# Kernel optimization log

Measured on AMD Instinct MI355X. Metric: run time of the kernel, lower is better.

## Reference

```python
import jax, jax.numpy as jnp
import numpy as np

B, H, S, D = 2, 12, 2048, 64


def setup_inputs() -> dict:
    key = jax.random.key(0)
    kq, kk, kv = jax.random.split(key, 3)
    q = jax.random.normal(kq, (B, H, S, D), dtype=jnp.float32)
    k = jax.random.normal(kk, (B, H, S, D), dtype=jnp.float32)
    v = jax.random.normal(kv, (B, H, S, D), dtype=jnp.float32)
    # causal mask: True = attend (keep), lower triangle
    mask = jnp.tril(jnp.ones((S, S), dtype=bool))
    return {"q": q, "k": k, "v": v, "mask": mask}


def reference(q, k, v, mask):
    dim = q.shape[-1]
    # [B,H,S,S] scores
    scores = jnp.einsum("bhqd,bhkd->bhqk", q, k) / jnp.sqrt(jnp.asarray(dim, q.dtype))
    # dynamic mask-direction logic from the original module:
    # if the mask is denser in the strict upper triangle, True means "mask out";
    # otherwise True means "keep".
    sq = mask.shape[-1]
    sample = mask.reshape(-1, sq, sq)[0]
    upper = jnp.triu(jnp.ones_like(sample, dtype=bool), k=1)
    flip = jnp.sum(sample & upper) > jnp.sum(sample & ~upper)
    keep = jnp.where(flip, ~mask, mask)  # True = keep
    neg_inf = jnp.asarray(-jnp.inf, scores.dtype)
    scores = jnp.where(keep, scores, neg_inf)
    weights = jax.nn.softmax(scores, axis=-1)
    # dropout with p_drop=0.0 is the identity
    return jnp.einsum("bhqk,bhkd->bhqd", weights, v)
```

## Files before the change

kernel.cpp:

```cpp
#include <hip/hip_runtime.h>
#include <hip/hip_bf16.h>


#define SEQ 2048
#define DH 64
#define NHEADS 24
#define BN 64
#define LDK 72
#define NSLOT (NHEADS * 16 * 4)
#define WS_FA14  ((size_t)NSLOT * 8192 * 2 + (size_t)NSLOT * 128 * 4)

typedef float f32x4 __attribute__((ext_vector_type(4)));
typedef __bf16 bf16x8 __attribute__((ext_vector_type(8)));
typedef __bf16 bf16x4 __attribute__((ext_vector_type(4)));

#if __has_builtin(__builtin_amdgcn_exp2f)
#define EXP2F(x) __builtin_amdgcn_exp2f(x)
#else
#define EXP2F(x) exp2f(x)
#endif

#define QSCALE 0.1803368801111204f

__global__ __launch_bounds__(256, 3)
void fa17_kernel(const float* __restrict__ q, const float* __restrict__ k,
                 const float* __restrict__ v,
                 __bf16* __restrict__ opart, float* __restrict__ lpart,
                 float* __restrict__ out)
{
    const int bx = blockIdx.x;
    const int xcd = bx & 7;
    const int sub = bx >> 3;
    const int bh = (sub / 40) * 8 + xcd;
    const int rem = 39 - (sub % 40);
    int mt2, st;
    if      (rem >= 36) { mt2 = 15; st = 36; }
    else if (rem >= 32) { mt2 = 14; st = 32; }
    else if (rem >= 28) { mt2 = 13; st = 28; }
    else if (rem >= 24) { mt2 = 12; st = 24; }
    else if (rem >= 21) { mt2 = 11; st = 21; }
    else if (rem >= 18) { mt2 = 10; st = 18; }
    else if (rem >= 15) { mt2 = 9;  st = 15; }
    else if (rem >= 12) { mt2 = 8;  st = 12; }
    else if (rem >= 10) { mt2 = 7;  st = 10; }
    else if (rem >= 8)  { mt2 = 6;  st = 8; }
    else if (rem >= 6)  { mt2 = 5;  st = 6; }
    else if (rem >= 4)  { mt2 = 4;  st = 4; }
    else                { mt2 = rem; st = rem; }
    const int chunk = rem - st;
    const int jt0 = chunk * 8;
    const int jt_end = min(jt0 + 8, 2 * mt2 + 2);
    const int q0 = mt2 * 128;

    const int tid = threadIdx.x;
    const int w = tid >> 6, lane = tid & 63;
    const int g = lane >> 4, li = lane & 15;

    __shared__ __bf16 Ks[2][4096];
    __shared__ __bf16 Vs[2][4096];
    __shared__ __bf16 Ps[4 * 32 * 64];

    const float* kh = k + (size_t)bh * SEQ * DH;
    const float* vh = v + (size_t)bh * SEQ * DH;

    bf16x8 qf[2][2];
    #pragma unroll
    for (int a = 0; a < 2; ++a) {
        const float* qp = q + (size_t)bh * SEQ * DH +
                          (size_t)(q0 + w * 32 + a * 16 + li) * DH + g * 8;
        #pragma unroll
        for (int c = 0; c < 2; ++c) {
            f32x4 x0 = *(const f32x4*)(qp + c * 32);
            f32x4 x1 = *(const f32x4*)(qp + c * 32 + 4);
            #pragma unroll
            for (int j = 0; j < 4; ++j) {
                qf[a][c][j]     = (__bf16)(x0[j] * QSCALE);
                qf[a][c][4 + j] = (__bf16)(x1[j] * QSCALE);
            }
        }
    }

    bf16x8 ones;
    #pragma unroll
    for (int j = 0; j < 8; ++j) ones[j] = (__bf16)1.0f;

    f32x4 acc[2][4] = {};
    f32x4 accl[2] = {};

    const int srow0 = tid >> 3;
    const int sg    = tid & 7;
    const int klg   = sg ^ (srow0 & 7);

    const int kb = ((tid & 7) << 2) | ((tid & 128) >> 2);
    const int dr = (tid & 120) >> 1;
    const int vc  = kb >> 5;
    const int vg  = (kb >> 3) & 3;
    const int vjh = (kb >> 2) & 1;
    const int vpp = dr >> 4;
    const int vS32 = ((dr >> 2) & 3) ^ vpp;
    const int vwb = (((vpp * 2 + vc) * 4 + vg) << 8) | (vS32 << 6) |
                    (vg << 4) | (vjh << 3);

    f32x4 ka[2][2], va[4];
    auto issueKV = [&](int jt) {
        const float* kp = kh + (size_t)(jt * BN + srow0) * DH + klg * 8;
        ka[0][0] = *(const f32x4*)kp;
        ka[0][1] = *(const f32x4*)(kp + 4);
        kp += 32 * DH;
        ka[1][0] = *(const f32x4*)kp;
        ka[1][1] = *(const f32x4*)(kp + 4);
        const float* vpx = vh + (size_t)(jt * BN + kb) * DH + dr;
        #pragma unroll
        for (int ii = 0; ii < 4; ++ii) va[ii] = *(const f32x4*)(vpx + ii * DH);
    };
    auto commitKV = [&](int b) {
        #pragma unroll
        for (int s = 0; s < 2; ++s) {
            bf16x8 o;
            #pragma unroll
            for (int jj = 0; jj < 4; ++jj) {
                o[jj]     = (__bf16)ka[s][0][jj];
                o[4 + jj] = (__bf16)ka[s][1][jj];
            }
            *(bf16x8*)((char*)Ks[b] + s * 4096 + tid * 16) = o;
        }
        #pragma unroll
        for (int dd = 0; dd < 4; ++dd) {
            bf16x4 p4v;
            #pragma unroll
            for (int ii = 0; ii < 4; ++ii) p4v[ii] = (__bf16)va[ii][dd];
            *(bf16x4*)((char*)Vs[b] + (vwb ^ (dd << 4))) = p4v;
        }
    };

    issueKV(jt0);
    commitKV(0);
    if (jt0 + 1 < jt_end) issueKV(jt0 + 1);
    __syncthreads();

    int buf = 0;
    for (int jt = jt0; jt < jt_end; ++jt) {
        if (jt + 1 < jt_end) commitKV(buf ^ 1);
        if (jt + 2 < jt_end) issueKV(jt + 2);

        const char* Kb = (const char*)Ks[buf];
        float s4[2][4][4];
        __builtin_amdgcn_s_setprio(1);
        #pragma unroll
        for (int t = 0; t < 4; ++t) {
            f32x4 sa0 = {}, sa1 = {};
            #pragma unroll
            for (int c = 0; c < 2; ++c) {
                bf16x8 kf = *(const bf16x8*)(Kb +
                    (t * 16 + li) * 128 + (((c * 4 + g) ^ (li & 7)) << 4));
                sa0 = __builtin_amdgcn_mfma_f32_16x16x32_bf16(kf, qf[0][c], sa0, 0, 0, 0);
                sa1 = __builtin_amdgcn_mfma_f32_16x16x32_bf16(kf, qf[1][c], sa1, 0, 0, 0);
            }
            #pragma unroll
            for (int r = 0; r < 4; ++r) { s4[0][t][r] = sa0[r]; s4[1][t][r] = sa1[r]; }
        }
        __builtin_amdgcn_s_setprio(0);

        if (jt >= 2 * mt2) {
            #pragma unroll
            for (int a = 0; a < 2; ++a) {
                const int qr = q0 + w * 32 + a * 16 + li;
                #pragma unroll
                for (int t = 0; t < 4; ++t) {
                    #pragma unroll
                    for (int r = 0; r < 4; ++r)
                        if (jt * 64 + t * 16 + g * 4 + r > qr) s4[a][t][r] = -1e30f;
                }
            }
        }

        #pragma unroll
        for (int a = 0; a < 2; ++a) {
            const int row = a * 16 + li;
            #pragma unroll
            for (int t = 0; t < 4; ++t) {
                bf16x4 p4;
                #pragma unroll
                for (int r = 0; r < 4; ++r) p4[r] = (__bf16)EXP2F(s4[a][t][r]);
                const int pg = (t * 2 + (g >> 1)) ^ (li & 7);
                *(bf16x4*)((char*)Ps + w * 4096 + row * 128 + (pg << 4) + ((g & 1) << 3)) = p4;
            }
        }

        __builtin_amdgcn_s_setprio(1);
        #pragma unroll
        for (int c = 0; c < 2; ++c) {
            const int pgp = ((c * 4 + g) ^ (li & 7)) << 4;
            bf16x8 pf0 = *(const bf16x8*)((const char*)Ps + w * 4096 + li * 128 + pgp);
            bf16x8 pf1 = *(const bf16x8*)((const char*)Ps + w * 4096 + (16 + li) * 128 + pgp);
            accl[0] = __builtin_amdgcn_mfma_f32_16x16x32_bf16(pf0, ones, accl[0], 0, 0, 0);
            accl[1] = __builtin_amdgcn_mfma_f32_16x16x32_bf16(pf1, ones, accl[1], 0, 0, 0);
            #pragma unroll
            for (int t = 0; t < 4; ++t) {
                bf16x8 vf = *(const bf16x8*)((const char*)Vs[buf] +
                    ((((t * 2 + c) * 4 + g) << 8) | ((li ^ (g | (t << 2))) << 4)));
                acc[0][t] = __builtin_amdgcn_mfma_f32_16x16x32_bf16(pf0, vf, acc[0][t], 0, 0, 0);
                acc[1][t] = __builtin_amdgcn_mfma_f32_16x16x32_bf16(pf1, vf, acc[1][t], 0, 0, 0);
            }
        }
        __builtin_amdgcn_s_setprio(0);

        if (jt + 1 < jt_end) __syncthreads();
        buf ^= 1;
    }

    if (2 * mt2 + 2 <= 8) {
        float* oh = out + (size_t)bh * SEQ * DH;
        #pragma unroll
        for (int a = 0; a < 2; ++a) {
            #pragma unroll
            for (int r = 0; r < 4; ++r) {
                const int row = q0 + w * 32 + a * 16 + g * 4 + r;
                const float inv = 1.0f / accl[a][r];
                float* op = oh + (size_t)row * DH + li;
                #pragma unroll
                for (int t = 0; t < 4; ++t) op[t * 16] = acc[a][t][r] * inv;
            }
        }
    } else {
        const int slot = (bh * 16 + mt2) * 4 + chunk;
        __bf16* po = opart + (size_t)slot * 8192;
        #pragma unroll
        for (int a = 0; a < 2; ++a) {
            #pragma unroll
            for (int r = 0; r < 4; ++r) {
                const int row = w * 32 + a * 16 + g * 4 + r;
                __bf16* op = po + row * 64 + li;
                #pragma unroll
                for (int t = 0; t < 4; ++t) op[t * 16] = (__bf16)acc[a][t][r];
                if (li == 0) lpart[(size_t)slot * 128 + row] = accl[a][r];
            }
        }
    }
}

__global__ __launch_bounds__(256)
void fa_reduce(const __bf16* __restrict__ opart, const float* __restrict__ lpart,
               float* __restrict__ out)
{
    const int bx = blockIdx.x;
    const int xcd = bx & 7;
    const int r2 = bx >> 3;
    const int bh = (r2 / 12) * 8 + xcd;
    const int mt2 = 4 + (r2 % 12);
    const int nc = (mt2 >> 2) + 1;
    const int base = (bh * 16 + mt2) * 4;
    const int tid = threadIdx.x;
    #pragma unroll
    for (int rnd = 0; rnd < 8; ++rnd) {
        const int flat = rnd * 1024 + tid * 4;
        const int row = flat >> 6;
        float o0 = 0, o1 = 0, o2 = 0, o3 = 0, l = 0;
        for (int c = 0; c < nc; ++c) {
            bf16x4 ov = *(const bf16x4*)(opart + (size_t)(base + c) * 8192 + flat);
            o0 += (float)ov[0]; o1 += (float)ov[1]; o2 += (float)ov[2]; o3 += (float)ov[3];
            l += lpart[(size_t)(base + c) * 128 + row];
        }
        const float inv = 1.0f / l;
        f32x4 res = { o0 * inv, o1 * inv, o2 * inv, o3 * inv };
        *(f32x4*)(out + (size_t)bh * SEQ * DH + (size_t)mt2 * 8192 + flat) = res;
    }
}

__global__ __launch_bounds__(256, 2)
void fa_causal_kernel(const float* __restrict__ q, const float* __restrict__ k,
                      const float* __restrict__ v, float* __restrict__ out)
{
    const int mt = 31 - (blockIdx.x & 31);
    const int bh = blockIdx.x >> 5;
    const int tid = threadIdx.x;
    const int w = tid >> 6, lane = tid & 63;
    const int g = lane >> 4, li = lane & 15;
    const int m0 = mt * 64;
    __shared__ __bf16 KsF[BN][LDK];
    __shared__ __bf16 VsF[DH][LDK];
    __shared__ __bf16 PsF[4][16][LDK];
    const size_t head_off = (size_t)bh * SEQ * DH;
    const float* qh = q + head_off;
    const float* kh = k + head_off;
    const float* vh = v + head_off;
    float* oh = out + head_off;
    const int qrow = m0 + w * 16 + li;
    bf16x8 qf[2];
    {
        const float* qp = qh + (size_t)qrow * DH + g * 8;
        #pragma unroll
        for (int c = 0; c < 2; ++c) {
            const float* p = qp + c * 32;
            #pragma unroll
            for (int jj = 0; jj < 8; ++jj) qf[c][jj] = (__bf16)p[jj];
        }
    }
    f32x4 acc[4] = {};
    float mrow[4], lrow[4];
    #pragma unroll
    for (int r = 0; r < 4; ++r) { mrow[r] = -1e30f; lrow[r] = 0.0f; }
    const float scale = 0.125f;
    const int srow = tid >> 2, scol = (tid & 3) * 16;
    for (int jt = 0; jt <= mt; ++jt) {
        const int kv0 = jt * BN;
        __syncthreads();
        {
            const float* kp = kh + (size_t)(kv0 + srow) * DH + scol;
            __bf16 tmp[16];
            #pragma unroll
            for (int jj = 0; jj < 16; ++jj) tmp[jj] = (__bf16)kp[jj];
            *(bf16x8*)&KsF[srow][scol]     = *(bf16x8*)&tmp[0];
            *(bf16x8*)&KsF[srow][scol + 8] = *(bf16x8*)&tmp[8];
            const float* vp = vh + (size_t)(kv0 + srow) * DH + scol;
            #pragma unroll
            for (int jj = 0; jj < 16; ++jj) VsF[scol + jj][srow] = (__bf16)vp[jj];
        }
        __syncthreads();
        float s4[4][4];
        #pragma unroll
        for (int t = 0; t < 4; ++t) {
            f32x4 sa = {};
            #pragma unroll
            for (int c = 0; c < 2; ++c) {
                bf16x8 kfr = *(const bf16x8*)&KsF[t * 16 + li][c * 32 + g * 8];
                sa = __builtin_amdgcn_mfma_f32_16x16x32_bf16(qf[c], kfr, sa, 0, 0, 0);
            }
            #pragma unroll
            for (int r = 0; r < 4; ++r) s4[t][r] = sa[r] * scale;
        }
        if (jt == mt) {
            #pragma unroll
            for (int t = 0; t < 4; ++t) {
                const int col = kv0 + t * 16 + li;
                #pragma unroll
                for (int r = 0; r < 4; ++r)
                    if (col > m0 + w * 16 + g * 4 + r) s4[t][r] = -1e30f;
            }
        }
        #pragma unroll
        for (int r = 0; r < 4; ++r) {
            float mx = fmaxf(fmaxf(s4[0][r], s4[1][r]), fmaxf(s4[2][r], s4[3][r]));
            #pragma unroll
            for (int off = 1; off < 16; off <<= 1)
                mx = fmaxf(mx, __shfl_xor(mx, off, 64));
            const float mnew = fmaxf(mrow[r], mx);
            const float alpha = __expf(mrow[r] - mnew);
            mrow[r] = mnew;
            float ps = 0.0f;
            #pragma unroll
            for (int t = 0; t < 4; ++t) {
                const float p = __expf(s4[t][r] - mnew);
                s4[t][r] = p;
                ps += p;
            }
            #pragma unroll
            for (int off = 1; off < 16; off <<= 1)
                ps += __shfl_xor(ps, off, 64);
            lrow[r] = lrow[r] * alpha + ps;
            #pragma unroll
            for (int t = 0; t < 4; ++t) acc[t][r] *= alpha;
        }
        #pragma unroll
        for (int t = 0; t < 4; ++t)
            #pragma unroll
            for (int r = 0; r < 4; ++r)
                PsF[w][g * 4 + r][t * 16 + li] = (__bf16)s4[t][r];
        __syncthreads();
        #pragma unroll
        for (int c = 0; c < 2; ++c) {
            bf16x8 pf = *(const bf16x8*)&PsF[w][li][c * 32 + g * 8];
            #pragma unroll
            for (int t = 0; t < 4; ++t) {
                bf16x8 vfr = *(const bf16x8*)&VsF[t * 16 + li][c * 32 + g * 8];
                acc[t] = __builtin_amdgcn_mfma_f32_16x16x32_bf16(pf, vfr, acc[t], 0, 0, 0);
            }
        }
    }
    #pragma unroll
    for (int r = 0; r < 4; ++r) {
        const int row = m0 + w * 16 + g * 4 + r;
        const float inv = 1.0f / lrow[r];
        float* op = oh + (size_t)row * DH + li;
        #pragma unroll
        for (int t = 0; t < 4; ++t) op[t * 16] = acc[t][r] * inv;
    }
}

extern "C" void kernel_launch(void* const* d_in, const int* in_sizes, int n_in,
                              void* d_out, int out_size, void* d_ws, size_t ws_size,
                              hipStream_t stream) {
    (void)in_sizes; (void)n_in; (void)out_size;
    const float* q = (const float*)d_in[0];
    const float* k = (const float*)d_in[1];
    const float* v = (const float*)d_in[2];
    float* out = (float*)d_out;

    if (ws_size >= WS_FA14) {
        __bf16* opart = (__bf16*)d_ws;
        float* lpart = (float*)((char*)d_ws + (size_t)NSLOT * 8192 * 2);
        fa17_kernel<<<dim3(960), dim3(256), 0, stream>>>(q, k, v, opart, lpart, out);
        fa_reduce<<<dim3(288), dim3(256), 0, stream>>>(opart, lpart, out);
    } else {
        fa_causal_kernel<<<dim3(NHEADS * 32), dim3(256), 0, stream>>>(q, k, v, out);
    }
}
```

Measured before the change: 127.7 us.

## Switch attention MFMAs to 32x32x16 and pass P through registers instead of LDS

Replaces the 16x16x32 bf16 MFMA tiling with 32x32x16 MFMAs for both QK^T and PV. Because of how the 32x32 layout lines up, the softmax probabilities can be repacked in registers with a cross-half lane shuffle, so the per-warp P round trip through shared memory goes away. The V tile is stored in LDS in a transposed, XOR-swizzled layout to match the new operand layout. Occupancy is raised to 4 blocks per CU. This lowers LDS traffic and instruction count, but risks register pressure from the larger f32x16 accumulators under the tighter launch bound.

```diff
diff --git a/kernel.cpp b/kernel.cpp
--- a/kernel.cpp
+++ b/kernel.cpp
@@ -11,8 +11,12 @@
 #define WS_FA14  ((size_t)NSLOT * 8192 * 2 + (size_t)NSLOT * 128 * 4)
 
 typedef float f32x4 __attribute__((ext_vector_type(4)));
+typedef float f32x16 __attribute__((ext_vector_type(16)));
 typedef __bf16 bf16x8 __attribute__((ext_vector_type(8)));
 typedef __bf16 bf16x4 __attribute__((ext_vector_type(4)));
+typedef unsigned int u32;
+typedef u32 u32x2 __attribute__((ext_vector_type(2)));
+typedef u32 u32x4 __attribute__((ext_vector_type(4)));
 
 #if __has_builtin(__builtin_amdgcn_exp2f)
 #define EXP2F(x) __builtin_amdgcn_exp2f(x)
@@ -22,8 +26,8 @@
 
 #define QSCALE 0.1803368801111204f
 
-__global__ __launch_bounds__(256, 3)
-void fa17_kernel(const float* __restrict__ q, const float* __restrict__ k,
+__global__ __launch_bounds__(256, 4)
+void fa18_kernel(const float* __restrict__ q, const float* __restrict__ k,
                  const float* __restrict__ v,
                  __bf16* __restrict__ opart, float* __restrict__ lpart,
                  float* __restrict__ out)
@@ -54,28 +58,28 @@
 
     const int tid = threadIdx.x;
     const int w = tid >> 6, lane = tid & 63;
-    const int g = lane >> 4, li = lane & 15;
+    const int l31 = lane & 31;
+    const int hb = lane >> 5;
+    const bool ish = (hb != 0);
 
     __shared__ __bf16 Ks[2][4096];
     __shared__ __bf16 Vs[2][4096];
-    __shared__ __bf16 Ps[4 * 32 * 64];
 
     const float* kh = k + (size_t)bh * SEQ * DH;
     const float* vh = v + (size_t)bh * SEQ * DH;
-
-    bf16x8 qf[2][2];
-    #pragma unroll
-    for (int a = 0; a < 2; ++a) {
-        const float* qp = q + (size_t)bh * SEQ * DH +
-                          (size_t)(q0 + w * 32 + a * 16 + li) * DH + g * 8;
-        #pragma unroll
-        for (int c = 0; c < 2; ++c) {
-            f32x4 x0 = *(const f32x4*)(qp + c * 32);
-            f32x4 x1 = *(const f32x4*)(qp + c * 32 + 4);
+    const int qg = q0 + w * 32 + l31;
+
+    bf16x8 qn[4];
+    {
+        const float* qp = q + (size_t)bh * SEQ * DH + (size_t)qg * DH + hb * 8;
+        #pragma unroll
+        for (int ks = 0; ks < 4; ++ks) {
+            f32x4 x0 = *(const f32x4*)(qp + 16 * ks);
+            f32x4 x1 = *(const f32x4*)(qp + 16 * ks + 4);
             #pragma unroll
             for (int j = 0; j < 4; ++j) {
-                qf[a][c][j]     = (__bf16)(x0[j] * QSCALE);
-                qf[a][c][4 + j] = (__bf16)(x1[j] * QSCALE);
+                qn[ks][j]     = (__bf16)(x0[j] * QSCALE);
+                qn[ks][4 + j] = (__bf16)(x1[j] * QSCALE);
             }
         }
     }
@@ -84,22 +88,15 @@
     #pragma unroll
     for (int j = 0; j < 8; ++j) ones[j] = (__bf16)1.0f;
 
-    f32x4 acc[2][4] = {};
-    f32x4 accl[2] = {};
+    f32x16 acc_o0 = {}, acc_o1 = {};
+    f32x16 accl = {};
 
     const int srow0 = tid >> 3;
     const int sg    = tid & 7;
     const int klg   = sg ^ (srow0 & 7);
 
-    const int kb = ((tid & 7) << 2) | ((tid & 128) >> 2);
-    const int dr = (tid & 120) >> 1;
-    const int vc  = kb >> 5;
-    const int vg  = (kb >> 3) & 3;
-    const int vjh = (kb >> 2) & 1;
-    const int vpp = dr >> 4;
-    const int vS32 = ((dr >> 2) & 3) ^ vpp;
-    const int vwb = (((vpp * 2 + vc) * 4 + vg) << 8) | (vS32 << 6) |
-                    (vg << 4) | (vjh << 3);
+    const int kb    = (tid & 7) * 4 + ((tid & 128) >> 2);
+    const int dbase = ((tid >> 3) & 15) * 4;
 
     f32x4 ka[2][2], va[4];
     auto issueKV = [&](int jt) {
@@ -109,7 +106,7 @@
         kp += 32 * DH;
         ka[1][0] = *(const f32x4*)kp;
         ka[1][1] = *(const f32x4*)(kp + 4);
-        const float* vpx = vh + (size_t)(jt * BN + kb) * DH + dr;
+        const float* vpx = vh + (size_t)(jt * BN + kb) * DH + dbase;
         #pragma unroll
         for (int ii = 0; ii < 4; ++ii) va[ii] = *(const f32x4*)(vpx + ii * DH);
     };
@@ -126,10 +123,12 @@
         }
         #pragma unroll
         for (int dd = 0; dd < 4; ++dd) {
+            const int d = dbase + dd;
             bf16x4 p4v;
             #pragma unroll
             for (int ii = 0; ii < 4; ++ii) p4v[ii] = (__bf16)va[ii][dd];
-            *(bf16x4*)((char*)Vs[b] + (vwb ^ (dd << 4))) = p4v;
+            *(bf16x4*)((char*)Vs[b] + d * 128 +
+                       ((((kb >> 3) ^ (d & 7)) << 4) | ((kb & 7) * 2))) = p4v;
         }
     };
 
@@ -144,64 +143,64 @@
         if (jt + 2 < jt_end) issueKV(jt + 2);
 
         const char* Kb = (const char*)Ks[buf];
-        float s4[2][4][4];
+        const char* Vb = (const char*)Vs[buf];
+        f32x16 sa0 = {}, sa1 = {};
         __builtin_amdgcn_s_setprio(1);
         #pragma unroll
-        for (int t = 0; t < 4; ++t) {
-            f32x4 sa0 = {}, sa1 = {};
-            #pragma unroll
-            for (int c = 0; c < 2; ++c) {
-                bf16x8 kf = *(const bf16x8*)(Kb +
-                    (t * 16 + li) * 128 + (((c * 4 + g) ^ (li & 7)) << 4));
-                sa0 = __builtin_amdgcn_mfma_f32_16x16x32_bf16(kf, qf[0][c], sa0, 0, 0, 0);
-                sa1 = __builtin_amdgcn_mfma_f32_16x16x32_bf16(kf, qf[1][c], sa1, 0, 0, 0);
-            }
-            #pragma unroll
-            for (int r = 0; r < 4; ++r) { s4[0][t][r] = sa0[r]; s4[1][t][r] = sa1[r]; }
+        for (int ks = 0; ks < 4; ++ks) {
+            bf16x8 kf0 = *(const bf16x8*)(Kb + l31 * 128 +
+                                          (((2 * ks + hb) ^ (lane & 7)) << 4));
+            bf16x8 kf1 = *(const bf16x8*)(Kb + (32 + l31) * 128 +
+                                          (((2 * ks + hb) ^ (lane & 7)) << 4));
+            sa0 = __builtin_amdgcn_mfma_f32_32x32x16_bf16(kf0, qn[ks], sa0, 0, 0, 0);
+            sa1 = __builtin_amdgcn_mfma_f32_32x32x16_bf16(kf1, qn[ks], sa1, 0, 0, 0);
         }
         __builtin_amdgcn_s_setprio(0);
 
         if (jt >= 2 * mt2) {
             #pragma unroll
-            for (int a = 0; a < 2; ++a) {
-                const int qr = q0 + w * 32 + a * 16 + li;
-                #pragma unroll
-                for (int t = 0; t < 4; ++t) {
-                    #pragma unroll
-                    for (int r = 0; r < 4; ++r)
-                        if (jt * 64 + t * 16 + g * 4 + r > qr) s4[a][t][r] = -1e30f;
-                }
-            }
-        }
-
-        #pragma unroll
-        for (int a = 0; a < 2; ++a) {
-            const int row = a * 16 + li;
-            #pragma unroll
-            for (int t = 0; t < 4; ++t) {
-                bf16x4 p4;
-                #pragma unroll
-                for (int r = 0; r < 4; ++r) p4[r] = (__bf16)EXP2F(s4[a][t][r]);
-                const int pg = (t * 2 + (g >> 1)) ^ (li & 7);
-                *(bf16x4*)((char*)Ps + w * 4096 + row * 128 + (pg << 4) + ((g & 1) << 3)) = p4;
-            }
+            for (int reg = 0; reg < 16; ++reg) {
+                const int kvr = jt * 64 + (reg & 3) + 8 * (reg >> 2) + 4 * hb;
+                if (kvr > qg)      sa0[reg] = -1e30f;
+                if (kvr + 32 > qg) sa1[reg] = -1e30f;
+            }
+        }
+
+        u32 pk[8][2];
+        #pragma unroll
+        for (int sp = 0; sp < 4; ++sp) {
+            bf16x4 qd0, qd1;
+            #pragma unroll
+            for (int r = 0; r < 4; ++r) {
+                qd0[r] = (__bf16)EXP2F(sa0[sp * 4 + r]);
+                qd1[r] = (__bf16)EXP2F(sa1[sp * 4 + r]);
+            }
+            u32x2 t0 = *(u32x2*)&qd0;
+            u32x2 t1 = *(u32x2*)&qd1;
+            pk[sp][0] = t0[0];     pk[sp][1] = t0[1];
+            pk[4 + sp][0] = t1[0]; pk[4 + sp][1] = t1[1];
         }
 
         __builtin_amdgcn_s_setprio(1);
         #pragma unroll
-        for (int c = 0; c < 2; ++c) {
-            const int pgp = ((c * 4 + g) ^ (li & 7)) << 4;
-            bf16x8 pf0 = *(const bf16x8*)((const char*)Ps + w * 4096 + li * 128 + pgp);
-            bf16x8 pf1 = *(const bf16x8*)((const char*)Ps + w * 4096 + (16 + li) * 128 + pgp);
-            accl[0] = __builtin_amdgcn_mfma_f32_16x16x32_bf16(pf0, ones, accl[0], 0, 0, 0);
-            accl[1] = __builtin_amdgcn_mfma_f32_16x16x32_bf16(pf1, ones, accl[1], 0, 0, 0);
-            #pragma unroll
-            for (int t = 0; t < 4; ++t) {
-                bf16x8 vf = *(const bf16x8*)((const char*)Vs[buf] +
-                    ((((t * 2 + c) * 4 + g) << 8) | ((li ^ (g | (t << 2))) << 4)));
-                acc[0][t] = __builtin_amdgcn_mfma_f32_16x16x32_bf16(pf0, vf, acc[0][t], 0, 0, 0);
-                acc[1][t] = __builtin_amdgcn_mfma_f32_16x16x32_bf16(pf1, vf, acc[1][t], 0, 0, 0);
-            }
+        for (int s = 0; s < 4; ++s) {
+            u32 sd0 = ish ? pk[2 * s][0] : pk[2 * s + 1][0];
+            u32 sd1 = ish ? pk[2 * s][1] : pk[2 * s + 1][1];
+            u32 r0 = (u32)__shfl_xor((int)sd0, 32, 64);
+            u32 r1 = (u32)__shfl_xor((int)sd1, 32, 64);
+            u32x4 wv;
+            wv[0] = ish ? r0 : pk[2 * s][0];
+            wv[1] = ish ? r1 : pk[2 * s][1];
+            wv[2] = ish ? pk[2 * s + 1][0] : r0;
+            wv[3] = ish ? pk[2 * s + 1][1] : r1;
+            bf16x8 pf = *(bf16x8*)&wv;
+            accl = __builtin_amdgcn_mfma_f32_32x32x16_bf16(pf, ones, accl, 0, 0, 0);
+            bf16x8 vf0 = *(const bf16x8*)(Vb + l31 * 128 +
+                                          (((2 * s + hb) ^ (lane & 7)) << 4));
+            bf16x8 vf1 = *(const bf16x8*)(Vb + (32 + l31) * 128 +
+                                          (((2 * s + hb) ^ (lane & 7)) << 4));
+            acc_o0 = __builtin_amdgcn_mfma_f32_32x32x16_bf16(pf, vf0, acc_o0, 0, 0, 0);
+            acc_o1 = __builtin_amdgcn_mfma_f32_32x32x16_bf16(pf, vf1, acc_o1, 0, 0, 0);
         }
         __builtin_amdgcn_s_setprio(0);
 
@@ -212,29 +211,21 @@
     if (2 * mt2 + 2 <= 8) {
         float* oh = out + (size_t)bh * SEQ * DH;
         #pragma unroll
-        for (int a = 0; a < 2; ++a) {
-            #pragma unroll
-            for (int r = 0; r < 4; ++r) {
-                const int row = q0 + w * 32 + a * 16 + g * 4 + r;
-                const float inv = 1.0f / accl[a][r];
-                float* op = oh + (size_t)row * DH + li;
-                #pragma unroll
-                for (int t = 0; t < 4; ++t) op[t * 16] = acc[a][t][r] * inv;
-            }
+        for (int reg = 0; reg < 16; ++reg) {
+            const int row = q0 + w * 32 + (reg & 3) + 8 * (reg >> 2) + 4 * hb;
+            const float inv = 1.0f / accl[reg];
+            oh[(size_t)row * DH + l31]      = acc_o0[reg] * inv;
+            oh[(size_t)row * DH + 32 + l31] = acc_o1[reg] * inv;
         }
     } else {
         const int slot = (bh * 16 + mt2) * 4 + chunk;
         __bf16* po = opart + (size_t)slot * 8192;
         #pragma unroll
-        for (int a = 0; a < 2; ++a) {
-            #pragma unroll
-            for (int r = 0; r < 4; ++r) {
-                const int row = w * 32 + a * 16 + g * 4 + r;
-                __bf16* op = po + row * 64 + li;
-                #pragma unroll
-                for (int t = 0; t < 4; ++t) op[t * 16] = (__bf16)acc[a][t][r];
-                if (li == 0) lpart[(size_t)slot * 128 + row] = accl[a][r];
-            }
+        for (int reg = 0; reg < 16; ++reg) {
+            const int row = w * 32 + (reg & 3) + 8 * (reg >> 2) + 4 * hb;
+            po[row * 64 + l31]      = (__bf16)acc_o0[reg];
+            po[row * 64 + 32 + l31] = (__bf16)acc_o1[reg];
+            if (l31 == 0) lpart[(size_t)slot * 128 + row] = accl[reg];
         }
     }
 }
@@ -399,7 +390,7 @@
     if (ws_size >= WS_FA14) {
         __bf16* opart = (__bf16*)d_ws;
         float* lpart = (float*)((char*)d_ws + (size_t)NSLOT * 8192 * 2);
-        fa17_kernel<<<dim3(960), dim3(256), 0, stream>>>(q, k, v, opart, lpart, out);
+        fa18_kernel<<<dim3(960), dim3(256), 0, stream>>>(q, k, v, opart, lpart, out);
         fa_reduce<<<dim3(288), dim3(256), 0, stream>>>(opart, lpart, out);
     } else {
         fa_causal_kernel<<<dim3(NHEADS * 32), dim3(256), 0, stream>>>(q, k, v, out);
```

Result: slower. 170.4 us (+33.4%).
